# Performance work log

Measured on AMD Instinct MI355X. Metric: run time of the kernel, lower is better.

Reference implementation:

```python
import jax, jax.numpy as jnp
import numpy as np

B, S = 10000, 32        # batch nodes, sampled neighbors per node
N, D_IN, D_H = 100000, 512, 512


def setup_inputs() -> dict:
    key = jax.random.key(0)
    k1, k2, k3 = jax.random.split(key, 3)
    neigh_idx = jax.random.randint(k1, (B, S), 0, N)                 # int neighbor ids
    features = jax.random.normal(k2, (N, D_IN), dtype=jnp.float32)   # node feature table
    W = jax.random.normal(k3, (D_H, D_IN), dtype=jnp.float32) * (1.0 / np.sqrt(D_IN))
    b = jnp.zeros((D_H,), dtype=jnp.float32)
    return {"neigh_idx": neigh_idx, "features": features, "W": W, "b": b}


def reference(neigh_idx, features, W, b):
    # gather neighbor embeddings: [B, S, D_IN]
    neigh_feats = features[neigh_idx]
    # MLP: Linear(input_dim, hidden_dim) + ReLU  -> [B, S, D_H]
    h = jax.nn.relu(jnp.einsum("bsd,hd->bsh", neigh_feats, W) + b)
    # mask-based mean pool over sampled neighbors (mask @ embed / row_sum) -> [B, D_H]
    return jnp.mean(h, axis=1)
```

## Files before the change

kernel.cpp:

```cpp
#include <hip/hip_runtime.h>
#include <hip/hip_bf16.h>


#define S_NB 32
#define D_IN 512
#define D_H  512
#define BM   128
#define BN   128
#define BK   32
#define NK   (D_IN / BK)
#define NNODE 100000
#define NBATCH 10000
#define NTILE_N 4
#define NTILE_M 784
#define NTILES  (NTILE_N * NTILE_M)

typedef __attribute__((ext_vector_type(8))) short  short8;
typedef __attribute__((ext_vector_type(4))) float  f32x4;
typedef __attribute__((ext_vector_type(4))) unsigned short us4;
typedef __attribute__((ext_vector_type(8))) unsigned short us8;

__device__ __forceinline__ unsigned short f2bf(float x) {
  union { float f; unsigned u; } v; v.f = x;
  unsigned r = v.u + 0x7FFFu + ((v.u >> 16) & 1u);
  return (unsigned short)(r >> 16);
}

__device__ __forceinline__ float bf2f(unsigned short x) {
  union { unsigned u; float f; } v; v.u = ((unsigned)x) << 16;
  return v.f;
}

__device__ __forceinline__ short8 cvt8bf(f32x4 lo, f32x4 hi) {
  union { __hip_bfloat162 h; unsigned u; } c0, c1, c2, c3;
  c0.h = __float22bfloat162_rn(make_float2(lo.x, lo.y));
  c1.h = __float22bfloat162_rn(make_float2(lo.z, lo.w));
  c2.h = __float22bfloat162_rn(make_float2(hi.x, hi.y));
  c3.h = __float22bfloat162_rn(make_float2(hi.z, hi.w));
  union { unsigned u[4]; short8 s; } r;
  r.u[0] = c0.u; r.u[1] = c1.u; r.u[2] = c2.u; r.u[3] = c3.u;
  return r.s;
}

__device__ __forceinline__ int swz(int row, int cb) {
  return row * 128 + (cb ^ ((row & 7) << 4));
}

__device__ __forceinline__ void gld_lds16(const void* g, void* l) {
  __builtin_amdgcn_global_load_lds(
      (const __attribute__((address_space(1))) unsigned int*)g,
      (__attribute__((address_space(3))) unsigned int*)l, 16, 0, 0);
}

__global__ __launch_bounds__(256, 8)
void cvt_bf16(const float* __restrict__ src, unsigned short* __restrict__ dst, int n8) {
  int i = blockIdx.x * blockDim.x + threadIdx.x;
  const int stride = gridDim.x * blockDim.x;
  for (; i < n8; i += stride) {
    f32x4 a = *(const f32x4*)(src + (size_t)i * 8);
    f32x4 b = *(const f32x4*)(src + (size_t)i * 8 + 4);
    us8 o;
    o[0] = f2bf(a.x); o[1] = f2bf(a.y); o[2] = f2bf(a.z); o[3] = f2bf(a.w);
    o[4] = f2bf(b.x); o[5] = f2bf(b.y); o[6] = f2bf(b.z); o[7] = f2bf(b.w);
    *(us8*)(dst + (size_t)i * 8) = o;
  }
}

__global__ __launch_bounds__(256, 3)
void gemm_f32a(const float* __restrict__ feat,
               const unsigned short* __restrict__ Wb,
               const float* __restrict__ bias,
               unsigned short* __restrict__ Hb) {
  const int tid  = threadIdx.x;
  const int lane = tid & 63;
  const int wid  = tid >> 6;
  const int wr   = wid >> 1;
  const int wc   = wid & 1;

  const int bid  = blockIdx.x;
  const int tile = (bid & 7) * (NTILES / 8) + (bid >> 3);
  const int n0   = (tile & 3) * BN;
  const int m0   = (tile >> 2) * BM;

  __shared__ __align__(16) float          As[2][BM * BK];
  __shared__ __align__(16) unsigned short Ws[2][64 * 64];

  const float* srcA[4];
  int dstAoff[4];
#pragma unroll
  for (int i = 0; i < 4; ++i) {
    int row = wid * 32 + i * 8 + (lane >> 3);
    int p   = lane & 7;
    int gr  = m0 + row; if (gr > NNODE - 1) gr = NNODE - 1;
    srcA[i]   = feat + (size_t)gr * D_IN + (p ^ (row & 7)) * 4;
    dstAoff[i] = (wid * 32 + i * 8) * BK;
  }

  const unsigned short* srcW[2];
  int dstWoff[2];
#pragma unroll
  for (int i = 0; i < 2; ++i) {
    int c = wid * 2 + i;
    int L = c * 8 + (lane >> 3);
    int p = lane & 7;
    int q = p ^ (L & 7);
    int rowbit = q >> 2, g0 = q & 3;
    srcW[i]   = Wb + (size_t)(n0 + L * 2 + rowbit) * D_IN + g0 * 8;
    dstWoff[i] = c * 512;
  }

  f32x4 acc[4][4];
#pragma unroll
  for (int i = 0; i < 4; ++i)
#pragma unroll
    for (int j = 0; j < 4; ++j)
      acc[i][j] = (f32x4){0.f, 0.f, 0.f, 0.f};

  const int frow = lane & 15;
  const int jg   = lane >> 4;
  const int arow = wr * 64 + frow;
  const int ag1 = ((2 * jg) ^ (frow & 7)) * 16;
  const int ag2 = ((2 * jg + 1) ^ (frow & 7)) * 16;
  const int wp  = ((((frow & 1) << 2) + jg) ^ ((frow >> 1) & 7)) * 16;
  const int wlb = wc * 32 + (frow >> 1);

#pragma unroll
  for (int i = 0; i < 4; ++i) gld_lds16(srcA[i], &As[0][dstAoff[i]]);
#pragma unroll
  for (int i = 0; i < 2; ++i) gld_lds16(srcW[i], &Ws[0][dstWoff[i]]);
  __syncthreads();

#pragma unroll
  for (int ki = 0; ki < NK; ++ki) {
    const int cur = ki & 1;

    if (ki < NK - 1) {
#pragma unroll
      for (int i = 0; i < 4; ++i)
        gld_lds16(srcA[i] + (ki + 1) * BK, &As[cur ^ 1][dstAoff[i]]);
#pragma unroll
      for (int i = 0; i < 2; ++i)
        gld_lds16(srcW[i] + (ki + 1) * BK, &Ws[cur ^ 1][dstWoff[i]]);
    }

    short8 af[4], bfr[4];
#pragma unroll
    for (int mi = 0; mi < 4; ++mi) {
      const char* base = (const char*)&As[cur][0] + (arow + mi * 16) * 128;
      f32x4 lo = *(const f32x4*)(base + ag1);
      f32x4 hi = *(const f32x4*)(base + ag2);
      af[mi] = cvt8bf(lo, hi);
    }
#pragma unroll
    for (int ni = 0; ni < 4; ++ni) {
      const char* base = (const char*)&Ws[cur][0] + (wlb + ni * 8) * 128;
      bfr[ni] = *(const short8*)(base + wp);
    }
#pragma unroll
    for (int mi = 0; mi < 4; ++mi)
#pragma unroll
      for (int ni = 0; ni < 4; ++ni)
        acc[mi][ni] = __builtin_amdgcn_mfma_f32_16x16x32_bf16(af[mi], bfr[ni], acc[mi][ni], 0, 0, 0);

    __syncthreads();
  }

  unsigned short* Cs = (unsigned short*)&As[0][0];
  const int rq = lane >> 4;
#pragma unroll
  for (int ni = 0; ni < 4; ++ni) {
    int col = wc * 64 + ni * 16 + frow;
    float bv = bias[n0 + col];
#pragma unroll
    for (int mi = 0; mi < 4; ++mi) {
#pragma unroll
      for (int r = 0; r < 4; ++r) {
        int row = wr * 64 + mi * 16 + rq * 4 + r;
        int byt = row * 256 + ((col * 2) ^ ((row & 7) << 4));
        *(unsigned short*)((char*)Cs + byt) = f2bf(fmaxf(acc[mi][ni][r] + bv, 0.f));
      }
    }
  }
  __syncthreads();

  const int srow = tid >> 4;
  const int scol = (tid & 15) * 8;
#pragma unroll
  for (int it = 0; it < 8; ++it) {
    int row  = it * 16 + srow;
    int grow = m0 + row;
    int byt  = row * 256 + (((tid & 15) * 16) ^ ((row & 7) << 4));
    us8 v = *(const us8*)((const char*)Cs + byt);
    if (grow < NNODE)
      *(us8*)(Hb + (size_t)grow * D_H + n0 + scol) = v;
  }
}

__global__ __launch_bounds__(256, 8)
void pool_mean4(const unsigned short* __restrict__ Hb,
                const int* __restrict__ nidx,
                float* __restrict__ out) {
  const int b4 = blockIdx.x;
  const int q  = threadIdx.x >> 6;
  const int t  = threadIdx.x & 63;
  const int b  = b4 * 4 + q;

  __shared__ int rows[4][S_NB];
  if (threadIdx.x < 4 * S_NB)
    rows[threadIdx.x >> 5][threadIdx.x & 31] = nidx[b4 * 4 * S_NB + threadIdx.x];
  __syncthreads();

  const int c = t * 8;
  float s0 = 0.f, s1 = 0.f, s2 = 0.f, s3 = 0.f;
  float s4 = 0.f, s5 = 0.f, s6 = 0.f, s7 = 0.f;
#pragma unroll
  for (int s = 0; s < S_NB; ++s) {
    us8 v = *(const us8*)(Hb + (size_t)rows[q][s] * D_H + c);
    s0 += bf2f(v[0]); s1 += bf2f(v[1]); s2 += bf2f(v[2]); s3 += bf2f(v[3]);
    s4 += bf2f(v[4]); s5 += bf2f(v[5]); s6 += bf2f(v[6]); s7 += bf2f(v[7]);
  }
  const float inv = 1.0f / (float)S_NB;
  f32x4 o1; o1.x = s0 * inv; o1.y = s1 * inv; o1.z = s2 * inv; o1.w = s3 * inv;
  f32x4 o2; o2.x = s4 * inv; o2.y = s5 * inv; o2.z = s6 * inv; o2.w = s7 * inv;
  *(f32x4*)(out + (size_t)b * D_H + c)     = o1;
  *(f32x4*)(out + (size_t)b * D_H + c + 4) = o2;
}

__global__ __launch_bounds__(256, 4)
void gemm_h(const float* __restrict__ feat,
            const float* __restrict__ Wm,
            const float* __restrict__ bias,
            unsigned short* __restrict__ Hb) {
  const int tid  = threadIdx.x;
  const int lane = tid & 63;
  const int wid  = tid >> 6;
  const int wr   = wid >> 1;
  const int wc   = wid & 1;
  const int n0   = blockIdx.x * BN;
  const int m0   = blockIdx.y * BM;

  __shared__ __align__(16) unsigned short As[BM * 64];
  __shared__ __align__(16) unsigned short Bs[BM * 64];

  const int lr = tid >> 4;
  const int lc = tid & 15;

  const float* aptr[8];
  const float* wptr[8];
#pragma unroll
  for (int p = 0; p < 8; ++p) {
    int row = p * 16 + lr;
    int gr  = m0 + row; if (gr > NNODE - 1) gr = NNODE - 1;
    aptr[p] = feat + (size_t)gr * D_IN + lc * 4;
    wptr[p] = Wm + (size_t)(n0 + row) * D_IN + lc * 4;
  }

  f32x4 acc[4][4];
#pragma unroll
  for (int i = 0; i < 4; ++i)
#pragma unroll
    for (int j = 0; j < 4; ++j)
      acc[i][j] = (f32x4){0.f, 0.f, 0.f, 0.f};

  const int frow = lane & 15;
  const int kcb  = (lane >> 4) * 16;
  const int arow = wr * 64 + frow;
  const int brow = wc * 64 + frow;

  for (int k0 = 0; k0 < D_IN; k0 += 64) {
    __syncthreads();
#pragma unroll
    for (int p = 0; p < 8; ++p) {
      int row = p * 16 + lr;
      f32x4 av = *(const f32x4*)(aptr[p] + k0);
      f32x4 wv = *(const f32x4*)(wptr[p] + k0);
      us4 a4, w4;
      a4.x = f2bf(av.x); a4.y = f2bf(av.y); a4.z = f2bf(av.z); a4.w = f2bf(av.w);
      w4.x = f2bf(wv.x); w4.y = f2bf(wv.y); w4.z = f2bf(wv.z); w4.w = f2bf(wv.w);
      *(us4*)((char*)As + swz(row, lc * 8)) = a4;
      *(us4*)((char*)Bs + swz(row, lc * 8)) = w4;
    }
    __syncthreads();

#pragma unroll
    for (int kk = 0; kk < 2; ++kk) {
      short8 af[4], bfr[4];
#pragma unroll
      for (int mi = 0; mi < 4; ++mi)
        af[mi] = *(const short8*)((const char*)As + swz(arow + mi * 16, kk * 64 + kcb));
#pragma unroll
      for (int ni = 0; ni < 4; ++ni)
        bfr[ni] = *(const short8*)((const char*)Bs + swz(brow + ni * 16, kk * 64 + kcb));
#pragma unroll
      for (int mi = 0; mi < 4; ++mi)
#pragma unroll
        for (int ni = 0; ni < 4; ++ni)
          acc[mi][ni] = __builtin_amdgcn_mfma_f32_16x16x32_bf16(af[mi], bfr[ni], acc[mi][ni], 0, 0, 0);
    }
  }

  const int rq = lane >> 4;
#pragma unroll
  for (int ni = 0; ni < 4; ++ni) {
    int col = n0 + wc * 64 + ni * 16 + frow;
    float bv = bias[col];
#pragma unroll
    for (int mi = 0; mi < 4; ++mi) {
#pragma unroll
      for (int r = 0; r < 4; ++r) {
        int grow = m0 + wr * 64 + mi * 16 + rq * 4 + r;
        if (grow < NNODE)
          Hb[(size_t)grow * D_H + col] = f2bf(fmaxf(acc[mi][ni][r] + bv, 0.f));
      }
    }
  }
}

__global__ __launch_bounds__(256, 4)
void pool_aggr_gemm(const int* __restrict__ nidx_g,
                    const float* __restrict__ feat,
                    const float* __restrict__ Wm,
                    const float* __restrict__ bias,
                    float* __restrict__ out) {
  const int tid  = threadIdx.x;
  const int lane = tid & 63;
  const int wid  = tid >> 6;
  const int wr   = wid >> 1;
  const int wc   = wid & 1;
  const int n0   = blockIdx.x * BN;
  const int mb   = blockIdx.y;

  __shared__ __align__(16) unsigned short As[BM * 64];
  __shared__ __align__(16) unsigned short Bs[BM * 64];
  __shared__ int nid[BM];

  if (tid < BM) nid[tid] = nidx_g[mb * BM + tid];
  __syncthreads();

  const int lr = tid >> 4;
  const int lc = tid & 15;

  const float* aptr[8];
  const float* wptr[8];
#pragma unroll
  for (int p = 0; p < 8; ++p) {
    int row = p * 16 + lr;
    aptr[p] = feat + (size_t)nid[row] * D_IN + lc * 4;
    wptr[p] = Wm + (size_t)(n0 + row) * D_IN + lc * 4;
  }

  f32x4 acc[4][4];
#pragma unroll
  for (int i = 0; i < 4; ++i)
#pragma unroll
    for (int j = 0; j < 4; ++j)
      acc[i][j] = (f32x4){0.f, 0.f, 0.f, 0.f};

  const int frow = lane & 15;
  const int kcb  = (lane >> 4) * 16;
  const int arow = wr * 64 + frow;
  const int brow = wc * 64 + frow;

  for (int k0 = 0; k0 < D_IN; k0 += 64) {
    __syncthreads();
#pragma unroll
    for (int p = 0; p < 8; ++p) {
      int row = p * 16 + lr;
      f32x4 av = *(const f32x4*)(aptr[p] + k0);
      f32x4 wv = *(const f32x4*)(wptr[p] + k0);
      us4 a4, w4;
      a4.x = f2bf(av.x); a4.y = f2bf(av.y); a4.z = f2bf(av.z); a4.w = f2bf(av.w);
      w4.x = f2bf(wv.x); w4.y = f2bf(wv.y); w4.z = f2bf(wv.z); w4.w = f2bf(wv.w);
      *(us4*)((char*)As + swz(row, lc * 8)) = a4;
      *(us4*)((char*)Bs + swz(row, lc * 8)) = w4;
    }
    __syncthreads();

#pragma unroll
    for (int kk = 0; kk < 2; ++kk) {
      short8 af[4], bfr[4];
#pragma unroll
      for (int mi = 0; mi < 4; ++mi)
        af[mi] = *(const short8*)((const char*)As + swz(arow + mi * 16, kk * 64 + kcb));
#pragma unroll
      for (int ni = 0; ni < 4; ++ni)
        bfr[ni] = *(const short8*)((const char*)Bs + swz(brow + ni * 16, kk * 64 + kcb));
#pragma unroll
      for (int mi = 0; mi < 4; ++mi)
#pragma unroll
        for (int ni = 0; ni < 4; ++ni)
          acc[mi][ni] = __builtin_amdgcn_mfma_f32_16x16x32_bf16(af[mi], bfr[ni], acc[mi][ni], 0, 0, 0);
    }
  }

  const int rq = lane >> 4;
#pragma unroll
  for (int ni = 0; ni < 4; ++ni) {
    int col = n0 + wc * 64 + ni * 16 + frow;
    float bv = bias[col];
#pragma unroll
    for (int bl = 0; bl < 2; ++bl) {
      float s = 0.f;
#pragma unroll
      for (int m2 = 0; m2 < 2; ++m2) {
        int mi = bl * 2 + m2;
#pragma unroll
        for (int r = 0; r < 4; ++r)
          s += fmaxf(acc[mi][ni][r] + bv, 0.f);
      }
      s += __shfl_xor(s, 16);
      s += __shfl_xor(s, 32);
      if (rq == 0) {
        int bb = mb * 4 + wr * 2 + bl;
        out[(size_t)bb * D_H + col] = s * (1.0f / (float)S_NB);
      }
    }
  }
}

extern "C" void kernel_launch(void* const* d_in, const int* in_sizes, int n_in,
                              void* d_out, int out_size, void* d_ws, size_t ws_size,
                              hipStream_t stream) {
  const int*   nidx = (const int*)d_in[0];
  const float* feat = (const float*)d_in[1];
  const float* Wm   = (const float*)d_in[2];
  const float* bias = (const float*)d_in[3];
  float* out = (float*)d_out;

  const size_t wb_elems = (size_t)D_H * D_IN;
  const size_t wb_bytes = wb_elems * sizeof(unsigned short);
  const size_t h_bytes  = (size_t)NNODE * D_H * sizeof(unsigned short);

  if (ws_size >= wb_bytes + h_bytes) {
    unsigned short* Wb = (unsigned short*)d_ws;
    unsigned short* Hb = Wb + wb_elems;
    cvt_bf16<<<128, 256, 0, stream>>>(Wm, Wb, D_H * D_IN / 8);
    gemm_f32a<<<NTILES, 256, 0, stream>>>(feat, Wb, bias, Hb);
    pool_mean4<<<NBATCH / 4, 256, 0, stream>>>(Hb, nidx, out);
  } else if (ws_size >= h_bytes) {
    unsigned short* Hb = (unsigned short*)d_ws;
    dim3 g1(D_H / BN, (NNODE + BM - 1) / BM);
    gemm_h<<<g1, 256, 0, stream>>>(feat, Wm, bias, Hb);
    pool_mean4<<<NBATCH / 4, 256, 0, stream>>>(Hb, nidx, out);
  } else {
    dim3 grid(D_H / BN, NBATCH / 4);
    pool_aggr_gemm<<<grid, 256, 0, stream>>>(nidx, feat, Wm, bias, out);
  }
}
```

Before: 191.8 us.

## Load GEMM A operand directly from global into registers, drop A LDS staging

The fp32 feature tile is no longer staged through shared memory with async global-to-LDS copies. Each lane now loads its MFMA fragment straight from global memory into registers and converts it to bf16 there. The LDS footprint shrinks to just the W double buffer, and the epilogue reuses that buffer in two half-passes. This is meant to raise occupancy (launch bounds go from 3 to 4 blocks) and remove the LDS round trip for A, at the cost of losing prefetch overlap for A and issuing less coalesced global loads (32-byte pieces per row) right before the MFMAs.

Result: slower. 309.2 us (+61.2%).

```diff
diff --git a/kernel.cpp b/kernel.cpp
--- a/kernel.cpp
+++ b/kernel.cpp
@@ -66,11 +66,11 @@
   }
 }
 
-__global__ __launch_bounds__(256, 3)
-void gemm_f32a(const float* __restrict__ feat,
-               const unsigned short* __restrict__ Wb,
-               const float* __restrict__ bias,
-               unsigned short* __restrict__ Hb) {
+__global__ __launch_bounds__(256, 4)
+void gemm_direct(const float* __restrict__ feat,
+                 const unsigned short* __restrict__ Wb,
+                 const float* __restrict__ bias,
+                 unsigned short* __restrict__ Hb) {
   const int tid  = threadIdx.x;
   const int lane = tid & 63;
   const int wid  = tid >> 6;
@@ -82,18 +82,17 @@
   const int n0   = (tile & 3) * BN;
   const int m0   = (tile >> 2) * BM;
 
-  __shared__ __align__(16) float          As[2][BM * BK];
   __shared__ __align__(16) unsigned short Ws[2][64 * 64];
 
-  const float* srcA[4];
-  int dstAoff[4];
-#pragma unroll
-  for (int i = 0; i < 4; ++i) {
-    int row = wid * 32 + i * 8 + (lane >> 3);
-    int p   = lane & 7;
-    int gr  = m0 + row; if (gr > NNODE - 1) gr = NNODE - 1;
-    srcA[i]   = feat + (size_t)gr * D_IN + (p ^ (row & 7)) * 4;
-    dstAoff[i] = (wid * 32 + i * 8) * BK;
+  const int frow = lane & 15;
+  const int jg   = lane >> 4;
+
+  const float* aptr[4];
+#pragma unroll
+  for (int mi = 0; mi < 4; ++mi) {
+    int row = m0 + wr * 64 + mi * 16 + frow;
+    if (row > NNODE - 1) row = NNODE - 1;
+    aptr[mi] = feat + (size_t)row * D_IN + jg * 8;
   }
 
   const unsigned short* srcW[2];
@@ -116,17 +115,10 @@
     for (int j = 0; j < 4; ++j)
       acc[i][j] = (f32x4){0.f, 0.f, 0.f, 0.f};
 
-  const int frow = lane & 15;
-  const int jg   = lane >> 4;
-  const int arow = wr * 64 + frow;
-  const int ag1 = ((2 * jg) ^ (frow & 7)) * 16;
-  const int ag2 = ((2 * jg + 1) ^ (frow & 7)) * 16;
   const int wp  = ((((frow & 1) << 2) + jg) ^ ((frow >> 1) & 7)) * 16;
   const int wlb = wc * 32 + (frow >> 1);
 
 #pragma unroll
-  for (int i = 0; i < 4; ++i) gld_lds16(srcA[i], &As[0][dstAoff[i]]);
-#pragma unroll
   for (int i = 0; i < 2; ++i) gld_lds16(srcW[i], &Ws[0][dstWoff[i]]);
   __syncthreads();
 
@@ -136,26 +128,25 @@
 
     if (ki < NK - 1) {
 #pragma unroll
-      for (int i = 0; i < 4; ++i)
-        gld_lds16(srcA[i] + (ki + 1) * BK, &As[cur ^ 1][dstAoff[i]]);
-#pragma unroll
       for (int i = 0; i < 2; ++i)
         gld_lds16(srcW[i] + (ki + 1) * BK, &Ws[cur ^ 1][dstWoff[i]]);
     }
 
-    short8 af[4], bfr[4];
+    short8 af[4];
 #pragma unroll
     for (int mi = 0; mi < 4; ++mi) {
-      const char* base = (const char*)&As[cur][0] + (arow + mi * 16) * 128;
-      f32x4 lo = *(const f32x4*)(base + ag1);
-      f32x4 hi = *(const f32x4*)(base + ag2);
+      f32x4 lo = *(const f32x4*)(aptr[mi] + ki * BK);
+      f32x4 hi = *(const f32x4*)(aptr[mi] + ki * BK + 4);
       af[mi] = cvt8bf(lo, hi);
     }
+
+    short8 bfr[4];
 #pragma unroll
     for (int ni = 0; ni < 4; ++ni) {
       const char* base = (const char*)&Ws[cur][0] + (wlb + ni * 8) * 128;
       bfr[ni] = *(const short8*)(base + wp);
     }
+
 #pragma unroll
     for (int mi = 0; mi < 4; ++mi)
 #pragma unroll
@@ -165,34 +156,38 @@
     __syncthreads();
   }
 
-  unsigned short* Cs = (unsigned short*)&As[0][0];
+  unsigned short* Cs = &Ws[0][0];
   const int rq = lane >> 4;
 #pragma unroll
-  for (int ni = 0; ni < 4; ++ni) {
-    int col = wc * 64 + ni * 16 + frow;
-    float bv = bias[n0 + col];
-#pragma unroll
-    for (int mi = 0; mi < 4; ++mi) {
-#pragma unroll
-      for (int r = 0; r < 4; ++r) {
-        int row = wr * 64 + mi * 16 + rq * 4 + r;
-        int byt = row * 256 + ((col * 2) ^ ((row & 7) << 4));
-        *(unsigned short*)((char*)Cs + byt) = f2bf(fmaxf(acc[mi][ni][r] + bv, 0.f));
+  for (int p = 0; p < 2; ++p) {
+    if (wr == p) {
+#pragma unroll
+      for (int ni = 0; ni < 4; ++ni) {
+        int col = wc * 64 + ni * 16 + frow;
+        float bv = bias[n0 + col];
+#pragma unroll
+        for (int mi = 0; mi < 4; ++mi) {
+#pragma unroll
+          for (int r = 0; r < 4; ++r) {
+            int lr = mi * 16 + rq * 4 + r;
+            int byt = lr * 256 + ((col * 2) ^ ((lr & 7) << 4));
+            *(unsigned short*)((char*)Cs + byt) = f2bf(fmaxf(acc[mi][ni][r] + bv, 0.f));
+          }
+        }
       }
     }
-  }
-  __syncthreads();
-
-  const int srow = tid >> 4;
-  const int scol = (tid & 15) * 8;
-#pragma unroll
-  for (int it = 0; it < 8; ++it) {
-    int row  = it * 16 + srow;
-    int grow = m0 + row;
-    int byt  = row * 256 + (((tid & 15) * 16) ^ ((row & 7) << 4));
-    us8 v = *(const us8*)((const char*)Cs + byt);
-    if (grow < NNODE)
-      *(us8*)(Hb + (size_t)grow * D_H + n0 + scol) = v;
+    __syncthreads();
+    const int scol = (tid & 15) * 8;
+#pragma unroll
+    for (int it = 0; it < 4; ++it) {
+      int lr   = it * 16 + (tid >> 4);
+      int grow = m0 + p * 64 + lr;
+      int byt  = lr * 256 + (((tid & 15) * 16) ^ ((lr & 7) << 4));
+      us8 v = *(const us8*)((const char*)Cs + byt);
+      if (grow < NNODE)
+        *(us8*)(Hb + (size_t)grow * D_H + n0 + scol) = v;
+    }
+    if (p == 0) __syncthreads();
   }
 }
 
@@ -435,7 +430,7 @@
     unsigned short* Wb = (unsigned short*)d_ws;
     unsigned short* Hb = Wb + wb_elems;
     cvt_bf16<<<128, 256, 0, stream>>>(Wm, Wb, D_H * D_IN / 8);
-    gemm_f32a<<<NTILES, 256, 0, stream>>>(feat, Wb, bias, Hb);
+    gemm_direct<<<NTILES, 256, 0, stream>>>(feat, Wb, bias, Hb);
     pool_mean4<<<NBATCH / 4, 256, 0, stream>>>(Hb, nidx, out);
   } else if (ws_size >= h_bytes) {
     unsigned short* Hb = (unsigned short*)d_ws;
```
